# Kernel optimization log

Measured on AMD Instinct MI355X. Metric: run time of the kernel, lower is better.

Reference implementation:

```python
import jax, jax.numpy as jnp
import numpy as np
from jax import lax


def _conv(x, w, b):
    out = lax.conv_general_dilated(x, w, (1, 1), [(0, 0), (0, 0)],
                                   dimension_numbers=('NCHW', 'OIHW', 'NCHW'))
    return out + b[None, :, None, None]


def _bn(x, g, b, eps=1e-5):
    # BatchNorm2d in training mode: biased batch statistics over (N,H,W)
    m = jnp.mean(x, axis=(0, 2, 3), keepdims=True)
    v = jnp.var(x, axis=(0, 2, 3), keepdims=True)
    return (x - m) * lax.rsqrt(v + eps) * g[None, :, None, None] + b[None, :, None, None]


def _maxpool2(x):
    return lax.reduce_window(x, -jnp.inf, lax.max, (1, 1, 2, 2), (1, 1, 2, 2), 'VALID')


def _topk_mask(x, k):
    # TopK module: keep the k largest-|.| channels per (b,h,w), zero the rest.
    a = jnp.abs(x)
    kth = lax.top_k(jnp.moveaxis(a, 1, -1), k)[0][..., -1]  # [B,H,W] k-th largest |x|
    return x * (a >= kth[:, None, :, :]).astype(x.dtype)


def _embiggen(x):
    # im2col 3x3 stride 1 valid, flattened channel-major (c, kh, kw) like
    # patch.contiguous().view(B,-1) in the torch loop, but fully vectorized.
    B, C, H, W = x.shape
    Ho, Wo = H - 2, W - 2
    patches = jnp.stack([x[:, :, i:i + Ho, j:j + Wo]
                         for i in range(3) for j in range(3)], axis=2)  # [B,C,9,Ho,Wo]
    return patches.reshape(B, C * 9, Ho, Wo)


def setup_inputs() -> dict:
    key = jax.random.key(0)
    ks = jax.random.split(key, 40)
    it = iter(range(40))

    def w(shape):
        fan_in = int(np.prod(shape[1:]))
        return (jax.random.normal(ks[next(it)], shape, jnp.float32)
                / np.float32(np.sqrt(fan_in)))

    def bias(n):
        return jax.random.normal(ks[next(it)], (n,), jnp.float32) * 0.01

    def gamma(n):
        return jax.random.uniform(ks[next(it)], (n,), jnp.float32, 0.5, 1.5)

    inp = {}
    inp['x'] = jax.random.normal(ks[next(it)], (256, 3, 32, 32), jnp.float32)
    inp['enc_w'] = w((256, 3, 3, 3)); inp['enc_b'] = bias(256)
    inp['dec_w'] = w((27, 256, 1, 1)); inp['dec_b'] = bias(27)
    inp['red_w'] = w((64, 256, 1, 1)); inp['red_b'] = bias(64)
    inp['bn1_g'] = gamma(64); inp['bn1_b'] = bias(64)
    inp['conv1_w'] = w((96, 64, 3, 3)); inp['conv1_b'] = bias(96)
    inp['bn2_g'] = gamma(96); inp['bn2_b'] = bias(96)
    inp['conv2_w'] = w((128, 96, 3, 3)); inp['conv2_b'] = bias(128)
    inp['bn3_g'] = gamma(128); inp['bn3_b'] = bias(128)
    inp['conv3_w'] = w((160, 128, 3, 3)); inp['conv3_b'] = bias(160)
    inp['bn4_g'] = gamma(160); inp['bn4_b'] = bias(160)
    inp['conv4_w'] = w((192, 160, 3, 3)); inp['conv4_b'] = bias(192)
    inp['bn5_g'] = gamma(192); inp['bn5_b'] = bias(192)
    inp['conv5_w'] = w((256, 192, 3, 3)); inp['conv5_b'] = bias(256)
    inp['bnc_g'] = gamma(256); inp['bnc_b'] = bias(256)
    inp['fc_w'] = w((100, 1024)); inp['fc_b'] = bias(100)
    inp['k'] = 32  # round(64 / k_div=2)
    return inp


def reference(x, enc_w, enc_b, dec_w, dec_b, red_w, red_b,
              bn1_g, bn1_b, conv1_w, conv1_b,
              bn2_g, bn2_b, conv2_w, conv2_b,
              bn3_g, bn3_b, conv3_w, conv3_b,
              bn4_g, bn4_b, conv4_w, conv4_b,
              bn5_g, bn5_b, conv5_w, conv5_b,
              bnc_g, bnc_b, fc_w, fc_b, k):
    # SparseCodingLayer_First (encoder+topk computed once; torch recomputes identically)
    s = _topk_mask(_conv(x, enc_w, enc_b), k)            # [B,256,30,30]
    dec = jax.nn.sigmoid(_conv(s, dec_w, dec_b))         # [B,27,30,30]
    target = lax.stop_gradient(_embiggen(x))             # detached im2col target
    aux_loss = jnp.mean((target - dec) ** 2)
    h = _conv(s, red_w, red_b)                           # [B,64,30,30]
    # Conv6 backbone
    h = _maxpool2(_conv(jax.nn.relu(_bn(h, bn1_g, bn1_b)), conv1_w, conv1_b))  # [B,96,14,14]
    h = _conv(jax.nn.relu(_bn(h, bn2_g, bn2_b)), conv2_w, conv2_b)             # [B,128,12,12]
    h = _conv(jax.nn.relu(_bn(h, bn3_g, bn3_b)), conv3_w, conv3_b)             # [B,160,10,10]
    h = _maxpool2(_conv(jax.nn.relu(_bn(h, bn4_g, bn4_b)), conv4_w, conv4_b))  # [B,192,4,4]
    h = _conv(jax.nn.relu(_bn(h, bn5_g, bn5_b)), conv5_w, conv5_b)             # [B,256,2,2]
    feat = lax.stop_gradient(h)  # usecase == 'pretrain': features detached
    f = _bn(feat, bnc_g, bnc_b).reshape(feat.shape[0], -1)  # [B,1024]
    logits = f @ fc_w.T + fc_b                               # [B,100]
    preds = jnp.argmax(logits, axis=1)
    return logits, preds, aux_loss
```

## Files before the change

### kernel.cpp

```cpp
#include <hip/hip_runtime.h>

#define DEV_INLINE __device__ __forceinline__
typedef unsigned long long ull;
typedef unsigned int u32;
typedef unsigned short u16;
typedef __attribute__((ext_vector_type(8))) short short8v;
typedef __attribute__((ext_vector_type(4))) float f32x4;

DEV_INLINE u32 rne16(float f){
  u32 u = __float_as_uint(f);
  return (u + 0x7fffu + ((u>>16)&1u)) >> 16;
}
DEV_INLINE u32 packsplit(float a){
  u32 h = rne16(a);
  float hf = __uint_as_float(h<<16);
  u32 l = rne16(a - hf);
  return h | (l<<16);
}
DEV_INLINE float unpackv(u32 w){
  return __uint_as_float(w<<16) + __uint_as_float(w & 0xffff0000u);
}

__global__ void prep_all(const float* __restrict__ enc_w, float* __restrict__ encTg,
                         const float* __restrict__ dec_w, float* __restrict__ decT,
                         const float* __restrict__ red_w, float* __restrict__ redT,
                         const float* __restrict__ fc_w,  float* __restrict__ fcT,
                         const float* __restrict__ c1w, u16* __restrict__ W1h, u16* __restrict__ W1l,
                         const float* __restrict__ c2w, u16* __restrict__ W2h, u16* __restrict__ W2l,
                         const float* __restrict__ c3w, u16* __restrict__ W3h, u16* __restrict__ W3l,
                         const float* __restrict__ c4w, u16* __restrict__ W4h, u16* __restrict__ W4l,
                         const float* __restrict__ c5w, u16* __restrict__ W5h, u16* __restrict__ W5l)
{
  const int b = blockIdx.x, t = threadIdx.x;
  auto t2 = [&](const float* A, float* AT, int R, int C, int base){
    int i = (b-base)*256 + t; if (i < R*C){ int r=i%R, c=i/R; AT[i] = A[r*C+c]; }
  };
  auto pk = [&](const float* W, u16* wh, u16* wl, int CIN, int COUT, int base){
    int TPI = CIN/32, KS = 9*TPI;
    int tid = (b-base)*256 + t;
    if (tid >= KS*COUT) return;
    int co = tid % COUT, ks = tid / COUT;
    int tap = ks/TPI, cib = (ks - tap*TPI)*32;
    u16* dh = wh + (size_t)tid*32;
    u16* dl = wl + (size_t)tid*32;
    for (int kl=0; kl<32; ++kl){
      float w = W[((size_t)(co*CIN + cib + kl))*9 + tap];
      u32 h = rne16(w);
      float hf = __uint_as_float(h<<16);
      u32 l = rne16(w - hf);
      dh[kl] = (u16)h; dl[kl] = (u16)l;
    }
  };
  if      (b < 27)  t2(enc_w, encTg, 256, 27, 0);
  else if (b < 54)  t2(dec_w, decT, 27, 256, 27);
  else if (b < 118) t2(red_w, redT, 64, 256, 54);
  else if (b < 518) t2(fc_w,  fcT, 100, 1024, 118);
  else if (b < 525) pk(c1w, W1h, W1l, 64, 96, 518);
  else if (b < 539) pk(c2w, W2h, W2l, 96, 128, 525);
  else if (b < 562) pk(c3w, W3h, W3l, 128, 160, 539);
  else if (b < 596) pk(c4w, W4h, W4l, 160, 192, 562);
  else              pk(c5w, W5h, W5l, 192, 256, 596);
}

__global__ __launch_bounds__(256, 4) void stage_a1(
    const float* __restrict__ encTg, const float* __restrict__ enc_b,
    const float* __restrict__ x, const int* __restrict__ kp,
    float* __restrict__ svg_v, unsigned char* __restrict__ svg_i)
{
  __shared__ float  rows[9*32];
  __shared__ float  svf[30*33];
  __shared__ unsigned char svi[30*33];

  const int t = threadIdx.x, oh = blockIdx.x, b = blockIdx.y;
  const int k = __builtin_amdgcn_readfirstlane(*kp);
  const int wid = t>>6, lane = t&63;
  const float4* encW4 = (const float4*)encTg;

  for (int e=t; e<288; e+=256){
    int ci = e/96, r = (e/32)%3, xx = e&31;
    rows[(ci*3+r)*32+xx] = x[((b*3+ci)*32 + (oh+r))*32 + xx];
  }
  for (int e=t; e<990; e+=256){ svf[e]=0.f; svi[e]=0; }
  __syncthreads();

  const float4 eb = ((const float4*)enc_b)[lane];

  auto cnt4 = [&](unsigned c, unsigned u0, unsigned u1, unsigned u2, unsigned u3)->int{
    return __popcll(__ballot(u0>=c)) + __popcll(__ballot(u1>=c))
         + __popcll(__ballot(u2>=c)) + __popcll(__ballot(u3>=c));
  };
  auto compact = [&](float v0,float v1,float v2,float v3,
                     unsigned u0,unsigned u1,unsigned u2,unsigned u3,
                     unsigned th, int pi){
    bool k0=u0>=th, k1=u1>=th, k2=u2>=th, k3=u3>=th;
    ull B0=__ballot(k0), B1=__ballot(k1), B2=__ballot(k2), B3=__ballot(k3);
    ull below=(1ull<<lane)-1ull;
    int n0=__popcll(B0), n1=__popcll(B1), n2=__popcll(B2);
    int o0=__popcll(B0&below);
    int o1=n0+__popcll(B1&below);
    int o2=n0+n1+__popcll(B2&below);
    int o3=n0+n1+n2+__popcll(B3&below);
    float* sf = &svf[pi*33]; unsigned char* si = &svi[pi*33];
    if (k0&&o0<32){ sf[o0]=v0; si[o0]=(unsigned char)(4*lane+0); }
    if (k1&&o1<32){ sf[o1]=v1; si[o1]=(unsigned char)(4*lane+1); }
    if (k2&&o2<32){ sf[o2]=v2; si[o2]=(unsigned char)(4*lane+2); }
    if (k3&&o3<32){ sf[o3]=v3; si[o3]=(unsigned char)(4*lane+3); }
  };

  for (int it=0; it<4; ++it){
    const int pr = wid*4 + it;
    if (pr >= 15) break;
    const int ow0 = 2*pr;

    float a0=eb.x,a1=eb.y,a2=eb.z,a3=eb.w;
    float c0=eb.x,c1=eb.y,c2=eb.z,c3=eb.w;
    #pragma unroll
    for (int ci=0; ci<3; ++ci)
      #pragma unroll
      for (int i=0;i<3;++i){
        const int rbase = (ci*3+i)*32 + ow0;
        float p0 = rows[rbase+0], p1 = rows[rbase+1];
        float p2 = rows[rbase+2], p3 = rows[rbase+3];
        float4 w0 = encW4[(ci*9+i*3+0)*64 + lane];
        float4 w1 = encW4[(ci*9+i*3+1)*64 + lane];
        float4 w2 = encW4[(ci*9+i*3+2)*64 + lane];
        a0=fmaf(w0.x,p0,a0); a1=fmaf(w0.y,p0,a1); a2=fmaf(w0.z,p0,a2); a3=fmaf(w0.w,p0,a3);
        c0=fmaf(w0.x,p1,c0); c1=fmaf(w0.y,p1,c1); c2=fmaf(w0.z,p1,c2); c3=fmaf(w0.w,p1,c3);
        a0=fmaf(w1.x,p1,a0); a1=fmaf(w1.y,p1,a1); a2=fmaf(w1.z,p1,a2); a3=fmaf(w1.w,p1,a3);
        c0=fmaf(w1.x,p2,c0); c1=fmaf(w1.y,p2,c1); c2=fmaf(w1.z,p2,c2); c3=fmaf(w1.w,p2,c3);
        a0=fmaf(w2.x,p2,a0); a1=fmaf(w2.y,p2,a1); a2=fmaf(w2.z,p2,a2); a3=fmaf(w2.w,p2,a3);
        c0=fmaf(w2.x,p3,c0); c1=fmaf(w2.y,p3,c1); c2=fmaf(w2.z,p3,c2); c3=fmaf(w2.w,p3,c3);
      }

    unsigned A0=__float_as_uint(a0)&0x7fffffffu, A1=__float_as_uint(a1)&0x7fffffffu;
    unsigned A2=__float_as_uint(a2)&0x7fffffffu, A3=__float_as_uint(a3)&0x7fffffffu;
    unsigned C0=__float_as_uint(c0)&0x7fffffffu, C1=__float_as_uint(c1)&0x7fffffffu;
    unsigned C2=__float_as_uint(c2)&0x7fffffffu, C3=__float_as_uint(c3)&0x7fffffffu;

    unsigned thA=0, thB=0;
    int dA=0, dB=0;
    for (int bit=30; bit>=0; --bit){
      if (!dA){
        unsigned c = thA | (1u<<bit);
        int n = cnt4(c,A0,A1,A2,A3);
        if (n>=k) thA=c;
        if (n==k) dA=1;
      }
      if (!dB){
        unsigned c = thB | (1u<<bit);
        int n = cnt4(c,C0,C1,C2,C3);
        if (n>=k) thB=c;
        if (n==k) dB=1;
      }
      if (dA & dB) break;
    }

    compact(a0,a1,a2,a3, A0,A1,A2,A3, thA, ow0);
    compact(c0,c1,c2,c3, C0,C1,C2,C3, thB, ow0+1);
  }
  __syncthreads();

  const size_t gbase = (size_t)b*900 + (size_t)oh*30;
  for (int e=t; e<960; e+=256){
    int jj = e/30, pi = e - jj*30;
    svg_v[(size_t)jj*230400 + gbase + pi] = svf[pi*33+jj];
    svg_i[(size_t)jj*230400 + gbase + pi] = svi[pi*33+jj];
  }
}

__global__ __launch_bounds__(256, 2) void stage_a2(
    const float* __restrict__ svg_v, const unsigned char* __restrict__ svg_i,
    const float* __restrict__ decT, const float* __restrict__ dec_b,
    const float* __restrict__ x, float* __restrict__ auxp)
{
  __shared__ __align__(16) float decl[256*28];
  __shared__ float redbuf[256];
  const int t = threadIdx.x;
  for (int e=t; e<6912; e+=256){
    int r = e/27, o = e - r*27;
    decl[r*28+o] = decT[e];
  }
  __syncthreads();

  const int pos = blockIdx.x*256 + t;
  const int b = pos/900, rem = pos - b*900;
  const int oh = rem/30, ow = rem - (rem/30)*30;

  float d[27];
  #pragma unroll
  for (int o=0;o<27;++o) d[o] = dec_b[o];
  for (int jj=0; jj<32; ++jj){
    float v  = svg_v[(size_t)jj*230400 + pos];
    int  idx = (int)svg_i[(size_t)jj*230400 + pos];
    const float4* wr4 = (const float4*)(decl + idx*28);
    float4 w0=wr4[0], w1=wr4[1], w2=wr4[2], w3=wr4[3], w4=wr4[4], w5=wr4[5], w6=wr4[6];
    d[0]=fmaf(v,w0.x,d[0]);  d[1]=fmaf(v,w0.y,d[1]);  d[2]=fmaf(v,w0.z,d[2]);  d[3]=fmaf(v,w0.w,d[3]);
    d[4]=fmaf(v,w1.x,d[4]);  d[5]=fmaf(v,w1.y,d[5]);  d[6]=fmaf(v,w1.z,d[6]);  d[7]=fmaf(v,w1.w,d[7]);
    d[8]=fmaf(v,w2.x,d[8]);  d[9]=fmaf(v,w2.y,d[9]);  d[10]=fmaf(v,w2.z,d[10]); d[11]=fmaf(v,w2.w,d[11]);
    d[12]=fmaf(v,w3.x,d[12]); d[13]=fmaf(v,w3.y,d[13]); d[14]=fmaf(v,w3.z,d[14]); d[15]=fmaf(v,w3.w,d[15]);
    d[16]=fmaf(v,w4.x,d[16]); d[17]=fmaf(v,w4.y,d[17]); d[18]=fmaf(v,w4.z,d[18]); d[19]=fmaf(v,w4.w,d[19]);
    d[20]=fmaf(v,w5.x,d[20]); d[21]=fmaf(v,w5.y,d[21]); d[22]=fmaf(v,w5.z,d[22]); d[23]=fmaf(v,w5.w,d[23]);
    d[24]=fmaf(v,w6.x,d[24]); d[25]=fmaf(v,w6.y,d[25]); d[26]=fmaf(v,w6.z,d[26]);
  }
  float acc = 0.f;
  #pragma unroll
  for (int o=0;o<27;++o){
    int ci = o/9, r2 = (o - ci*9)/3, c2 = o%3;
    float tg = x[((b*3+ci)*32 + (oh+r2))*32 + (ow+c2)];
    float dv = 1.f/(1.f + __expf(-d[o]));
    float df = tg - dv;
    acc = fmaf(df, df, acc);
  }
  redbuf[t]=acc; __syncthreads();
  for (int off=128; off; off>>=1){ if (t<off) redbuf[t]+=redbuf[t+off]; __syncthreads(); }
  if (t==0) auxp[blockIdx.x] = redbuf[0];
}

__global__ __launch_bounds__(256) void stage_a3p2(
    const float* __restrict__ svg_v, const unsigned char* __restrict__ svg_i,
    const float* __restrict__ redT, const float* __restrict__ red_b,
    u32* __restrict__ x1p, float* __restrict__ psum1, float* __restrict__ psq1)
{
  __shared__ __align__(16) float redl[256*68];
  __shared__ u32   obuf[256*65];
  const int t = threadIdx.x;
  for (int e=t; e<16384; e+=256) redl[(e>>6)*68 + (e&63)] = redT[e];
  __syncthreads();

  const int pos = blockIdx.x*256 + t;

  float v[32]; int a[32];
  #pragma unroll
  for (int j=0;j<32;++j) v[j] = svg_v[(size_t)j*230400 + pos];
  #pragma unroll
  for (int j=0;j<32;++j) a[j] = (int)svg_i[(size_t)j*230400 + pos]*17;

  const float4* redl4 = (const float4*)redl;
  #pragma unroll 2
  for (int ocb=0; ocb<16; ++ocb){
    float s0 = red_b[4*ocb+0], s1 = red_b[4*ocb+1];
    float s2 = red_b[4*ocb+2], s3 = red_b[4*ocb+3];
    #pragma unroll
    for (int j=0;j<32;++j){
      float4 w = redl4[a[j] + ocb];
      s0 = fmaf(v[j], w.x, s0); s1 = fmaf(v[j], w.y, s1);
      s2 = fmaf(v[j], w.z, s2); s3 = fmaf(v[j], w.w, s3);
    }
    obuf[t*65 + 4*ocb+0] = packsplit(s0);
    obuf[t*65 + 4*ocb+1] = packsplit(s1);
    obuf[t*65 + 4*ocb+2] = packsplit(s2);
    obuf[t*65 + 4*ocb+3] = packsplit(s3);
  }
  __syncthreads();

  const size_t base = (size_t)blockIdx.x*16384;
  float s = 0.f, q = 0.f;
  for (int e=t; e<16384; e+=256){
    u32 w = obuf[(e>>6)*65 + (e&63)];
    x1p[base + e] = w;
    float vv = unpackv(w);
    s += vv; q = fmaf(vv, vv, q);
  }
  float* ls = redl; float* lq = redl + 256;
  ls[t] = s; lq[t] = q; __syncthreads();
  if (t < 128){ ls[t] += ls[t+128]; lq[t] += lq[t+128]; } __syncthreads();
  if (t < 64){
    psum1[(size_t)blockIdx.x*64 + t] = ls[t] + ls[t+64];
    psq1 [(size_t)blockIdx.x*64 + t] = lq[t] + lq[t+64];
  }
}

__global__ __launch_bounds__(256) void bn1_final(
    const float* __restrict__ ps, const float* __restrict__ pq,
    const float* __restrict__ g, const float* __restrict__ b2,
    float* __restrict__ sc, float* __restrict__ sh)
{
  __shared__ float ls[256], lq[256];
  const int c = blockIdx.x, t = threadIdx.x;
  float s=0.f, q=0.f;
  for (int i=t; i<900; i+=256){ s += ps[(size_t)i*64+c]; q += pq[(size_t)i*64+c]; }
  ls[t]=s; lq[t]=q; __syncthreads();
  for (int off=128; off; off>>=1){
    if (t<off){ ls[t]+=ls[t+off]; lq[t]+=lq[t+off]; } __syncthreads();
  }
  if (t==0){
    constexpr float inv_n = 1.f/230400.f;
    float m = ls[0]*inv_n;
    float var = fmaf(lq[0], inv_n, -m*m);
    float rs = rsqrtf(var + 1e-5f);
    float scale = g[c]*rs;
    sc[c] = scale;
    sh[c] = fmaf(-m, scale, b2[c]);
  }
}

template<int C>
__global__ __launch_bounds__(256) void bn_finalG(
    const float* __restrict__ ps, const float* __restrict__ pq, int G,
    const float* __restrict__ g, const float* __restrict__ b2,
    float* __restrict__ sc, float* __restrict__ sh, float inv_n)
{
  __shared__ float ls[256], lq[256];
  const int c = blockIdx.x, t = threadIdx.x;
  float s=0.f, q=0.f;
  for (int i=t; i<G; i+=256){ s += ps[(size_t)i*C+c]; q += pq[(size_t)i*C+c]; }
  ls[t]=s; lq[t]=q; __syncthreads();
  for (int off=128; off; off>>=1){
    if (t<off){ ls[t]+=ls[t+off]; lq[t]+=lq[t+off]; } __syncthreads();
  }
  if (t==0){
    float m = ls[0]*inv_n;
    float var = fmaf(lq[0], inv_n, -m*m);
    float rs = rsqrtf(var + 1e-5f);
    float scale = g[c]*rs;
    sc[c] = scale;
    sh[c] = fmaf(-m, scale, b2[c]);
  }
}

template<int C>
__global__ void cvt_repack(u32* __restrict__ xp, const float* __restrict__ sc,
                           const float* __restrict__ sh, int total4){
  int i = blockIdx.x*256 + threadIdx.x;
  if (i >= total4) return;
  uint4* p = (uint4*)xp;
  uint4 w = p[i];
  int cb = (i*4) % C;
  w.x = packsplit(fmaxf(fmaf(unpackv(w.x), sc[cb+0], sh[cb+0]), 0.f));
  w.y = packsplit(fmaxf(fmaf(unpackv(w.y), sc[cb+1], sh[cb+1]), 0.f));
  w.z = packsplit(fmaxf(fmaf(unpackv(w.z), sc[cb+2], sh[cb+2]), 0.f));
  w.w = packsplit(fmaxf(fmaf(unpackv(w.w), sc[cb+3], sh[cb+3]), 0.f));
  p[i] = w;
}

template<int CIN,int COUT,int HIN,int WIN,int BM,int MW,bool POOL,bool PKOUT>
__global__ __launch_bounds__(256) void conv_mfma(
    const u32* __restrict__ xp, const u16* __restrict__ wh,
    const u16* __restrict__ wl, const float* __restrict__ bias,
    void* __restrict__ y_, float* __restrict__ psC, float* __restrict__ qsC)
{
  constexpr int HC=HIN-2, WC=WIN-2, TPI=CIN/32, KS=9*TPI, NCH=COUT/16;
  const int t = threadIdx.x, wid = t>>6, lane = t&63;
  const int p0 = blockIdx.x*BM;
  const int colg = lane>>4;
  const int col = lane&15;
  float* yf = (float*)y_;
  u32*   yp = (u32*)y_;

  const u32* Aptr[MW];
  #pragma unroll
  for (int m=0;m<MW;++m){
    int l = (wid*MW+m)*16 + col;
    int lc = l < BM ? l : BM-1;
    int p = p0 + lc;
    int b = p/(HC*WC); int rem = p - b*(HC*WC);
    int oh = rem/WC, ow = rem - (rem/WC)*WC;
    Aptr[m] = xp + ((size_t)((b*HIN+oh)*WIN+ow))*CIN + colg*8;
  }
  const size_t wb = (size_t)col*32 + colg*8;

  f32x4 acc[MW][NCH];
  #pragma unroll
  for (int m=0;m<MW;++m)
    #pragma unroll
    for (int nc=0;nc<NCH;++nc) acc[m][nc] = (f32x4){0.f,0.f,0.f,0.f};

  for (int ks=0; ks<KS; ++ks){
    const int tap = ks/TPI, cib = (ks - tap*TPI)*32;
    const int kh = tap/3, kw = tap - kh*3;
    short8v ah[MW], al[MW];
    #pragma unroll
    for (int m=0;m<MW;++m){
      const u32* ap = Aptr[m] + (kh*WIN + kw)*CIN + cib;
      uint4 qa = *(const uint4*)(ap);
      uint4 qb = *(const uint4*)(ap+4);
      ah[m][0]=(short)(qa.x&0xffffu); al[m][0]=(short)(qa.x>>16);
      ah[m][1]=(short)(qa.y&0xffffu); al[m][1]=(short)(qa.y>>16);
      ah[m][2]=(short)(qa.z&0xffffu); al[m][2]=(short)(qa.z>>16);
      ah[m][3]=(short)(qa.w&0xffffu); al[m][3]=(short)(qa.w>>16);
      ah[m][4]=(short)(qb.x&0xffffu); al[m][4]=(short)(qb.x>>16);
      ah[m][5]=(short)(qb.y&0xffffu); al[m][5]=(short)(qb.y>>16);
      ah[m][6]=(short)(qb.z&0xffffu); al[m][6]=(short)(qb.z>>16);
      ah[m][7]=(short)(qb.w&0xffffu); al[m][7]=(short)(qb.w>>16);
    }
    const u16* whp = wh + (size_t)ks*COUT*32 + wb;
    const u16* wlp = wl + (size_t)ks*COUT*32 + wb;
    #pragma unroll
    for (int nc=0;nc<NCH;++nc){
      short8v bh = *(const short8v*)(whp + nc*512);
      short8v bl = *(const short8v*)(wlp + nc*512);
      #pragma unroll
      for (int m=0;m<MW;++m){
        acc[m][nc] = __builtin_amdgcn_mfma_f32_16x16x32_bf16(ah[m], bh, acc[m][nc], 0,0,0);
        acc[m][nc] = __builtin_amdgcn_mfma_f32_16x16x32_bf16(ah[m], bl, acc[m][nc], 0,0,0);
        acc[m][nc] = __builtin_amdgcn_mfma_f32_16x16x32_bf16(al[m], bh, acc[m][nc], 0,0,0);
      }
    }
  }

  if constexpr (!POOL){
    __shared__ float ldsS[4][COUT], ldsQ[4][COUT];
    float sacc[NCH], qacc[NCH];
    #pragma unroll
    for (int nc=0;nc<NCH;++nc){ sacc[nc]=0.f; qacc[nc]=0.f; }
    #pragma unroll
    for (int m=0;m<MW;++m){
      const int lr0 = (wid*MW+m)*16 + colg*4;
      #pragma unroll
      for (int nc=0;nc<NCH;++nc){
        float bv = bias[nc*16+col];
        #pragma unroll
        for (int r=0;r<4;++r)
          if (lr0+r < BM){
            float ov = acc[m][nc][r] + bv;
            float vv;
            if constexpr (PKOUT){
              u32 w = packsplit(ov);
              yp[(size_t)(p0+lr0+r)*COUT + nc*16+col] = w;
              vv = unpackv(w);
            } else {
              yf[(size_t)(p0+lr0+r)*COUT + nc*16+col] = ov;
              vv = ov;
            }
            sacc[nc] += vv; qacc[nc] = fmaf(vv, vv, qacc[nc]);
          }
      }
    }
    #pragma unroll
    for (int nc=0;nc<NCH;++nc){
      float s_ = sacc[nc], q_ = qacc[nc];
      s_ += __shfl_xor(s_, 16); q_ += __shfl_xor(q_, 16);
      s_ += __shfl_xor(s_, 32); q_ += __shfl_xor(q_, 32);
      if (colg == 0){ ldsS[wid][nc*16+col] = s_; ldsQ[wid][nc*16+col] = q_; }
    }
    __syncthreads();
    if (t < COUT){
      psC[(size_t)blockIdx.x*COUT + t] = ldsS[0][t]+ldsS[1][t]+ldsS[2][t]+ldsS[3][t];
      qsC[(size_t)blockIdx.x*COUT + t] = ldsQ[0][t]+ldsQ[1][t]+ldsQ[2][t]+ldsQ[3][t];
    }
  } else {
    constexpr int LDC = COUT+4;
    __shared__ float lds[BM*LDC];
    #pragma unroll
    for (int m=0;m<MW;++m){
      const int lr0 = (wid*MW+m)*16 + colg*4;
      #pragma unroll
      for (int nc=0;nc<NCH;++nc){
        float bv = bias[nc*16+col];
        #pragma unroll
        for (int r=0;r<4;++r)
          if (lr0+r < BM) lds[(lr0+r)*LDC + nc*16+col] = acc[m][nc][r] + bv;
      }
    }
    __syncthreads();
    constexpr int WPO = WC/2;
    const size_t pbase = (size_t)p0/4;
    if (t < COUT){
      float s = 0.f, q = 0.f;
      for (int pl=0; pl<BM/4; ++pl){
        int poh = pl / WPO, pw = pl - poh*WPO;
        int r = (2*poh)*WC + 2*pw;
        float mx = fmaxf(fmaxf(lds[r*LDC+t],      lds[(r+1)*LDC+t]),
                         fmaxf(lds[(r+WC)*LDC+t], lds[(r+WC+1)*LDC+t]));
        float vv;
        if constexpr (PKOUT){
          u32 w = packsplit(mx);
          yp[(pbase + pl)*COUT + t] = w;
          vv = unpackv(w);
        } else {
          yf[(pbase + pl)*COUT + t] = mx;
          vv = mx;
        }
        s += vv; q = fmaf(vv, vv, q);
      }
      psC[(size_t)blockIdx.x*COUT + t] = s;
      qsC[(size_t)blockIdx.x*COUT + t] = q;
    }
  }
}

__global__ __launch_bounds__(256) void fc_kernel(
    const float* __restrict__ a5, const float* __restrict__ scale, const float* __restrict__ shift,
    const float* __restrict__ fcT, const float* __restrict__ fc_b,
    const float* __restrict__ auxp, float* __restrict__ outp)
{
  const int b = blockIdx.x, t = threadIdx.x;
  if (b == 256){
    __shared__ float s[256];
    float a=0.f;
    for (int i=t; i<900; i+=256) a += auxp[i];
    s[t]=a; __syncthreads();
    for (int off=128; off; off>>=1){ if (t<off) s[t]+=s[t+off]; __syncthreads(); }
    if (t==0) outp[25856] = s[0] / 6220800.0f;
    return;
  }
  __shared__ float f[1024];
  __shared__ float part[256];
  __shared__ float lg[128];
  for (int e=t; e<1024; e+=256){
    int c = e & 255, hw = e >> 8;
    float v = a5[b*1024 + e];
    f[c*4 + hw] = fmaf(v, scale[c], shift[c]);
  }
  __syncthreads();
  const int o = t & 127, half = t >> 7;
  float s = 0.f;
  if (o < 100){
    const float* fp = f + half*512;
    const float* wp = fcT + half*512*100 + o;
    for (int j=0;j<512;++j) s = fmaf(fp[j], wp[j*100], s);
  }
  part[t] = s; __syncthreads();
  if (t < 128){
    float logit = part[t] + part[t+128] + ((t<100)? fc_b[t] : 0.f);
    lg[t] = (t<100)? logit : -3.0e38f;
    if (t<100) outp[b*100 + t] = logit;
  }
  __syncthreads();
  if (t==0){
    float m = lg[0]; int mi = 0;
    for (int i=1;i<100;++i){ if (lg[i] > m){ m = lg[i]; mi = i; } }
    outp[25600 + b] = (float)mi;
  }
}

extern "C" void kernel_launch(void* const* d_in, const int* in_sizes, int n_in,
                              void* d_out, int out_size, void* d_ws, size_t ws_size,
                              hipStream_t stream)
{
  (void)in_sizes; (void)n_in; (void)out_size;
  const float* x     = (const float*)d_in[0];
  const float* enc_w = (const float*)d_in[1];
  const float* enc_b = (const float*)d_in[2];
  const float* dec_w = (const float*)d_in[3];
  const float* dec_b = (const float*)d_in[4];
  const float* red_w = (const float*)d_in[5];
  const float* red_b = (const float*)d_in[6];
  const float* bn1_g = (const float*)d_in[7];  const float* bn1_b = (const float*)d_in[8];
  const float* c1w   = (const float*)d_in[9];  const float* c1b   = (const float*)d_in[10];
  const float* bn2_g = (const float*)d_in[11]; const float* bn2_b = (const float*)d_in[12];
  const float* c2w   = (const float*)d_in[13]; const float* c2b   = (const float*)d_in[14];
  const float* bn3_g = (const float*)d_in[15]; const float* bn3_b = (const float*)d_in[16];
  const float* c3w   = (const float*)d_in[17]; const float* c3b   = (const float*)d_in[18];
  const float* bn4_g = (const float*)d_in[19]; const float* bn4_b = (const float*)d_in[20];
  const float* c4w   = (const float*)d_in[21]; const float* c4b   = (const float*)d_in[22];
  const float* bn5_g = (const float*)d_in[23]; const float* bn5_b = (const float*)d_in[24];
  const float* c5w   = (const float*)d_in[25]; const float* c5b   = (const float*)d_in[26];
  const float* bnc_g = (const float*)d_in[27]; const float* bnc_b = (const float*)d_in[28];
  const float* fc_w  = (const float*)d_in[29]; const float* fc_b  = (const float*)d_in[30];
  const int*   kp    = (const int*)d_in[31];
  float* out = (float*)d_out;
  float* ws  = (float*)d_ws;

  constexpr size_t OFF_ENCT = 0;
  constexpr size_t OFF_DECT = 7168;
  constexpr size_t OFF_REDT = 14336;
  constexpr size_t OFF_FCT  = 30720;
  constexpr size_t OFF_W1H = 133120, OFF_W1L = 160768;
  constexpr size_t OFF_W2H = 188416, OFF_W2L = 243712;
  constexpr size_t OFF_W3H = 299008, OFF_W3L = 391168;
  constexpr size_t OFF_W4H = 483328, OFF_W4L = 621568;
  constexpr size_t OFF_W5H = 759808, OFF_W5L = 980992;
  constexpr size_t OFF_SS1 = 1202176, OFF_SS2 = 1202304, OFF_SS3 = 1202496;
  constexpr size_t OFF_SS4 = 1202752, OFF_SS5 = 1203072, OFF_SSC = 1203456;
  constexpr size_t OFF_AUX  = 1302272;
  constexpr size_t OFF_B    = 1303296;
  constexpr size_t OFF_C    = 16048896;
  constexpr size_t OFF_P1S  = 25264896;
  constexpr size_t OFF_P1Q  = OFF_P1S + 57600;
  constexpr size_t OFF_PCS  = OFF_P1Q + 57600;
  constexpr size_t OFF_PCQ  = OFF_PCS + 172032;
  constexpr size_t TOTALF   = OFF_PCQ + 172032;
  if (ws_size < TOTALF*sizeof(float)) return;

  float* encTg = ws + OFF_ENCT;
  float* decT = ws + OFF_DECT; float* redT = ws + OFF_REDT; float* fcT = ws + OFF_FCT;
  u16* W1h = (u16*)(ws+OFF_W1H); u16* W1l = (u16*)(ws+OFF_W1L);
  u16* W2h = (u16*)(ws+OFF_W2H); u16* W2l = (u16*)(ws+OFF_W2L);
  u16* W3h = (u16*)(ws+OFF_W3H); u16* W3l = (u16*)(ws+OFF_W3L);
  u16* W4h = (u16*)(ws+OFF_W4H); u16* W4l = (u16*)(ws+OFF_W4L);
  u16* W5h = (u16*)(ws+OFF_W5H); u16* W5l = (u16*)(ws+OFF_W5L);
  float* ss1 = ws+OFF_SS1; float* ss2 = ws+OFF_SS2; float* ss3 = ws+OFF_SS3;
  float* ss4 = ws+OFF_SS4; float* ss5 = ws+OFF_SS5; float* ssc = ws+OFF_SSC;
  float* auxp = ws+OFF_AUX;
  float* psum1 = ws+OFF_P1S; float* psq1 = ws+OFF_P1Q;
  float* pcs = ws+OFF_PCS;  float* pcq = ws+OFF_PCQ;
  u32*   x1p = (u32*)(ws+OFF_B);
  u32*   y2p = (u32*)(ws+OFF_B);
  u32*   p4p = (u32*)(ws+OFF_B);
  float* svv = ws+OFF_C;
  unsigned char* svi = (unsigned char*)(ws+OFF_C+7372800);
  u32*   p1p = (u32*)(ws+OFF_C);
  u32*   y3p = (u32*)(ws+OFF_C);
  float* y5  = ws+OFF_C;

  prep_all<<<650, 256, 0, stream>>>(enc_w, encTg, dec_w, decT, red_w, redT, fc_w, fcT,
                                    c1w, W1h, W1l, c2w, W2h, W2l, c3w, W3h, W3l,
                                    c4w, W4h, W4l, c5w, W5h, W5l);

  stage_a1<<<dim3(30,256), 256, 0, stream>>>(encTg, enc_b, x, kp, svv, svi);
  stage_a2<<<900, 256, 0, stream>>>(svv, svi, decT, dec_b, x, auxp);
  stage_a3p2<<<900, 256, 0, stream>>>(svv, svi, redT, red_b, x1p, psum1, psq1);

  bn1_final<<<64, 256, 0, stream>>>(psum1, psq1, bn1_g, bn1_b, ss1, ss1+64);
  cvt_repack<64><<<14400, 256, 0, stream>>>(x1p, ss1, ss1+64, 3686400);

  conv_mfma<64,96,30,30,112,2,true,true><<<1792, 256, 0, stream>>>(x1p, W1h, W1l, c1b, p1p, pcs, pcq);
  bn_finalG<96><<<96, 256, 0, stream>>>(pcs, pcq, 1792, bn2_g, bn2_b, ss2, ss2+96, 1.f/50176.f);
  cvt_repack<96><<<(1204224+255)/256, 256, 0, stream>>>(p1p, ss2, ss2+96, 1204224);

  conv_mfma<96,128,14,14,128,2,false,true><<<288, 256, 0, stream>>>(p1p, W2h, W2l, c2b, y2p, pcs, pcq);
  bn_finalG<128><<<128, 256, 0, stream>>>(pcs, pcq, 288, bn3_g, bn3_b, ss3, ss3+128, 1.f/36864.f);
  cvt_repack<128><<<(1179648+255)/256, 256, 0, stream>>>(y2p, ss3, ss3+128, 1179648);

  conv_mfma<128,160,12,12,128,2,false,true><<<200, 256, 0, stream>>>(y2p, W3h, W3l, c3b, y3p, pcs, pcq);
  bn_finalG<160><<<160, 256, 0, stream>>>(pcs, pcq, 200, bn4_g, bn4_b, ss4, ss4+160, 1.f/25600.f);
  cvt_repack<160><<<(1024000+255)/256, 256, 0, stream>>>(y3p, ss4, ss4+160, 1024000);

  conv_mfma<160,192,10,10,64,1,true,true><<<256, 256, 0, stream>>>(y3p, W4h, W4l, c4b, p4p, pcs, pcq);
  bn_finalG<192><<<192, 256, 0, stream>>>(pcs, pcq, 256, bn5_g, bn5_b, ss5, ss5+192, 1.f/4096.f);
  cvt_repack<192><<<(196608+255)/256, 256, 0, stream>>>(p4p, ss5, ss5+192, 196608);

  conv_mfma<192,256,4,4,64,1,false,false><<<16, 256, 0, stream>>>(p4p, W5h, W5l, c5b, y5, pcs, pcq);
  bn_finalG<256><<<256, 256, 0, stream>>>(pcs, pcq, 16, bnc_g, bnc_b, ssc, ssc+256, 1.f/1024.f);
  fc_kernel<<<257, 256, 0, stream>>>(y5, ssc, ssc+256, fcT, fc_b, auxp, out);
}
```

Measured before the change: 1.115 ms.

## Fuse decoder aux-loss computation into top-k stage, dropping separate stage_a2 kernel

The sparse decoder (1x1 conv over the top-k compacted activations), the sigmoid, and the squared-error against the im2col target now run at the end of stage_a1, reading the compacted values from shared memory instead of a separate kernel re-reading them from global memory. Decoder weights are pre-transposed into a padded 28-wide layout and loaded into shared memory in every stage_a1 block, and the aux partial sums grow to one per (batch,row), reduced later. This removes one launch and a global read pass over the sparse buffers. In exchange, stage_a1 uses about 28KB more shared memory, which may lower its occupancy, and each of its 7680 blocks reloads the decoder weights.

New measurement: 1.241 ms. 11.3% more time.

```diff
diff --git a/kernel.cpp b/kernel.cpp
--- a/kernel.cpp
+++ b/kernel.cpp
@@ -22,7 +22,7 @@
 }
 
 __global__ void prep_all(const float* __restrict__ enc_w, float* __restrict__ encTg,
-                         const float* __restrict__ dec_w, float* __restrict__ decT,
+                         const float* __restrict__ dec_w, float* __restrict__ decT28,
                          const float* __restrict__ red_w, float* __restrict__ redT,
                          const float* __restrict__ fc_w,  float* __restrict__ fcT,
                          const float* __restrict__ c1w, u16* __restrict__ W1h, u16* __restrict__ W1l,
@@ -51,25 +51,32 @@
       dh[kl] = (u16)h; dl[kl] = (u16)l;
     }
   };
-  if      (b < 27)  t2(enc_w, encTg, 256, 27, 0);
-  else if (b < 54)  t2(dec_w, decT, 27, 256, 27);
-  else if (b < 118) t2(red_w, redT, 64, 256, 54);
-  else if (b < 518) t2(fc_w,  fcT, 100, 1024, 118);
-  else if (b < 525) pk(c1w, W1h, W1l, 64, 96, 518);
-  else if (b < 539) pk(c2w, W2h, W2l, 96, 128, 525);
-  else if (b < 562) pk(c3w, W3h, W3l, 128, 160, 539);
-  else if (b < 596) pk(c4w, W4h, W4l, 160, 192, 562);
-  else              pk(c5w, W5h, W5l, 192, 256, 596);
+  if      (b < 27){
+    int i = b*256 + t;
+    if (i < 27*256){ int o = i/256, idx = i - o*256; decT28[idx*28 + o] = dec_w[i]; }
+  }
+  if      (b >= 27 && b < 54)  t2(enc_w, encTg, 256, 27, 27);
+  else if (b >= 54 && b < 118) t2(red_w, redT, 64, 256, 54);
+  else if (b >= 118 && b < 518) t2(fc_w,  fcT, 100, 1024, 118);
+  else if (b >= 518 && b < 525) pk(c1w, W1h, W1l, 64, 96, 518);
+  else if (b >= 525 && b < 539) pk(c2w, W2h, W2l, 96, 128, 525);
+  else if (b >= 539 && b < 562) pk(c3w, W3h, W3l, 128, 160, 539);
+  else if (b >= 562 && b < 596) pk(c4w, W4h, W4l, 160, 192, 562);
+  else if (b >= 596)            pk(c5w, W5h, W5l, 192, 256, 596);
 }
 
 __global__ __launch_bounds__(256, 4) void stage_a1(
     const float* __restrict__ encTg, const float* __restrict__ enc_b,
     const float* __restrict__ x, const int* __restrict__ kp,
-    float* __restrict__ svg_v, unsigned char* __restrict__ svg_i)
+    const float* __restrict__ decT28, const float* __restrict__ dec_b,
+    float* __restrict__ svg_v, unsigned char* __restrict__ svg_i,
+    float* __restrict__ auxp)
 {
   __shared__ float  rows[9*32];
   __shared__ float  svf[30*33];
   __shared__ unsigned char svi[30*33];
+  __shared__ __align__(16) float decl[256*28];
+  __shared__ float redbuf[256];
 
   const int t = threadIdx.x, oh = blockIdx.x, b = blockIdx.y;
   const int k = __builtin_amdgcn_readfirstlane(*kp);
@@ -81,6 +88,7 @@
     rows[(ci*3+r)*32+xx] = x[((b*3+ci)*32 + (oh+r))*32 + xx];
   }
   for (int e=t; e<990; e+=256){ svf[e]=0.f; svi[e]=0; }
+  for (int e=t; e<7168; e+=256) decl[e] = decT28[e];
   __syncthreads();
 
   const float4 eb = ((const float4*)enc_b)[lane];
@@ -166,54 +174,37 @@
     svg_v[(size_t)jj*230400 + gbase + pi] = svf[pi*33+jj];
     svg_i[(size_t)jj*230400 + gbase + pi] = svi[pi*33+jj];
   }
-}
-
-__global__ __launch_bounds__(256, 2) void stage_a2(
-    const float* __restrict__ svg_v, const unsigned char* __restrict__ svg_i,
-    const float* __restrict__ decT, const float* __restrict__ dec_b,
-    const float* __restrict__ x, float* __restrict__ auxp)
-{
-  __shared__ __align__(16) float decl[256*28];
-  __shared__ float redbuf[256];
-  const int t = threadIdx.x;
-  for (int e=t; e<6912; e+=256){
-    int r = e/27, o = e - r*27;
-    decl[r*28+o] = decT[e];
-  }
-  __syncthreads();
-
-  const int pos = blockIdx.x*256 + t;
-  const int b = pos/900, rem = pos - b*900;
-  const int oh = rem/30, ow = rem - (rem/30)*30;
-
-  float d[27];
-  #pragma unroll
-  for (int o=0;o<27;++o) d[o] = dec_b[o];
-  for (int jj=0; jj<32; ++jj){
-    float v  = svg_v[(size_t)jj*230400 + pos];
-    int  idx = (int)svg_i[(size_t)jj*230400 + pos];
-    const float4* wr4 = (const float4*)(decl + idx*28);
-    float4 w0=wr4[0], w1=wr4[1], w2=wr4[2], w3=wr4[3], w4=wr4[4], w5=wr4[5], w6=wr4[6];
-    d[0]=fmaf(v,w0.x,d[0]);  d[1]=fmaf(v,w0.y,d[1]);  d[2]=fmaf(v,w0.z,d[2]);  d[3]=fmaf(v,w0.w,d[3]);
-    d[4]=fmaf(v,w1.x,d[4]);  d[5]=fmaf(v,w1.y,d[5]);  d[6]=fmaf(v,w1.z,d[6]);  d[7]=fmaf(v,w1.w,d[7]);
-    d[8]=fmaf(v,w2.x,d[8]);  d[9]=fmaf(v,w2.y,d[9]);  d[10]=fmaf(v,w2.z,d[10]); d[11]=fmaf(v,w2.w,d[11]);
-    d[12]=fmaf(v,w3.x,d[12]); d[13]=fmaf(v,w3.y,d[13]); d[14]=fmaf(v,w3.z,d[14]); d[15]=fmaf(v,w3.w,d[15]);
-    d[16]=fmaf(v,w4.x,d[16]); d[17]=fmaf(v,w4.y,d[17]); d[18]=fmaf(v,w4.z,d[18]); d[19]=fmaf(v,w4.w,d[19]);
-    d[20]=fmaf(v,w5.x,d[20]); d[21]=fmaf(v,w5.y,d[21]); d[22]=fmaf(v,w5.z,d[22]); d[23]=fmaf(v,w5.w,d[23]);
-    d[24]=fmaf(v,w6.x,d[24]); d[25]=fmaf(v,w6.y,d[25]); d[26]=fmaf(v,w6.z,d[26]);
-  }
-  float acc = 0.f;
-  #pragma unroll
-  for (int o=0;o<27;++o){
-    int ci = o/9, r2 = (o - ci*9)/3, c2 = o%3;
-    float tg = x[((b*3+ci)*32 + (oh+r2))*32 + (ow+c2)];
-    float dv = 1.f/(1.f + __expf(-d[o]));
-    float df = tg - dv;
-    acc = fmaf(df, df, acc);
-  }
-  redbuf[t]=acc; __syncthreads();
+
+  float auxacc = 0.f;
+  if (t < 210){
+    const int pi = t/7, c = t - (t/7)*7;
+    const float4* decl4 = (const float4*)decl;
+    float av0=0.f, av1=0.f, av2=0.f, av3=0.f;
+    #pragma unroll
+    for (int j=0;j<32;++j){
+      float v = svf[pi*33+j];
+      int idx = (int)svi[pi*33+j];
+      float4 w = decl4[idx*7 + c];
+      av0 = fmaf(v, w.x, av0); av1 = fmaf(v, w.y, av1);
+      av2 = fmaf(v, w.z, av2); av3 = fmaf(v, w.w, av3);
+    }
+    float av[4] = {av0, av1, av2, av3};
+    #pragma unroll
+    for (int oj=0;oj<4;++oj){
+      int o = c*4 + oj;
+      if (o < 27){
+        float dacc = av[oj] + dec_b[o];
+        float dv = 1.f/(1.f + __expf(-dacc));
+        int ci = o/9, r2 = (o - ci*9)/3, c2 = o%3;
+        float tg = rows[(ci*3+r2)*32 + pi + c2];
+        float df = tg - dv;
+        auxacc = fmaf(df, df, auxacc);
+      }
+    }
+  }
+  redbuf[t] = auxacc; __syncthreads();
   for (int off=128; off; off>>=1){ if (t<off) redbuf[t]+=redbuf[t+off]; __syncthreads(); }
-  if (t==0) auxp[blockIdx.x] = redbuf[0];
+  if (t==0) auxp[(size_t)b*30 + oh] = redbuf[0];
 }
 
 __global__ __launch_bounds__(256) void stage_a3p2(
@@ -488,7 +479,7 @@
   if (b == 256){
     __shared__ float s[256];
     float a=0.f;
-    for (int i=t; i<900; i+=256) a += auxp[i];
+    for (int i=t; i<7680; i+=256) a += auxp[i];
     s[t]=a; __syncthreads();
     for (int off=128; off; off>>=1){ if (t<off) s[t]+=s[t+off]; __syncthreads(); }
     if (t==0) outp[25856] = s[0] / 6220800.0f;
@@ -563,18 +554,18 @@
   constexpr size_t OFF_W5H = 759808, OFF_W5L = 980992;
   constexpr size_t OFF_SS1 = 1202176, OFF_SS2 = 1202304, OFF_SS3 = 1202496;
   constexpr size_t OFF_SS4 = 1202752, OFF_SS5 = 1203072, OFF_SSC = 1203456;
-  constexpr size_t OFF_AUX  = 1302272;
   constexpr size_t OFF_B    = 1303296;
   constexpr size_t OFF_C    = 16048896;
   constexpr size_t OFF_P1S  = 25264896;
   constexpr size_t OFF_P1Q  = OFF_P1S + 57600;
   constexpr size_t OFF_PCS  = OFF_P1Q + 57600;
   constexpr size_t OFF_PCQ  = OFF_PCS + 172032;
-  constexpr size_t TOTALF   = OFF_PCQ + 172032;
+  constexpr size_t OFF_AUX  = OFF_PCQ + 172032;
+  constexpr size_t TOTALF   = OFF_AUX + 7680;
   if (ws_size < TOTALF*sizeof(float)) return;
 
   float* encTg = ws + OFF_ENCT;
-  float* decT = ws + OFF_DECT; float* redT = ws + OFF_REDT; float* fcT = ws + OFF_FCT;
+  float* decT28 = ws + OFF_DECT; float* redT = ws + OFF_REDT; float* fcT = ws + OFF_FCT;
   u16* W1h = (u16*)(ws+OFF_W1H); u16* W1l = (u16*)(ws+OFF_W1L);
   u16* W2h = (u16*)(ws+OFF_W2H); u16* W2l = (u16*)(ws+OFF_W2L);
   u16* W3h = (u16*)(ws+OFF_W3H); u16* W3l = (u16*)(ws+OFF_W3L);
@@ -594,12 +585,11 @@
   u32*   y3p = (u32*)(ws+OFF_C);
   float* y5  = ws+OFF_C;
 
-  prep_all<<<650, 256, 0, stream>>>(enc_w, encTg, dec_w, decT, red_w, redT, fc_w, fcT,
+  prep_all<<<650, 256, 0, stream>>>(enc_w, encTg, dec_w, decT28, red_w, redT, fc_w, fcT,
                                     c1w, W1h, W1l, c2w, W2h, W2l, c3w, W3h, W3l,
                                     c4w, W4h, W4l, c5w, W5h, W5l);
 
-  stage_a1<<<dim3(30,256), 256, 0, stream>>>(encTg, enc_b, x, kp, svv, svi);
-  stage_a2<<<900, 256, 0, stream>>>(svv, svi, decT, dec_b, x, auxp);
+  stage_a1<<<dim3(30,256), 256, 0, stream>>>(encTg, enc_b, x, kp, decT28, dec_b, svv, svi, auxp);
   stage_a3p2<<<900, 256, 0, stream>>>(svv, svi, redT, red_b, x1p, psum1, psq1);
 
   bn1_final<<<64, 256, 0, stream>>>(psum1, psq1, bn1_g, bn1_b, ss1, ss1+64);
```
